# Performance work log

Hardware: AMD Instinct MI355X
Metric: run time of the kernel (lower is better)

## Reference

```python
import jax, jax.numpy as jnp
import numpy as np

D_MODEL = 1024
NUM_HEADS = 16
D_HEAD = D_MODEL // NUM_HEADS
BATCH = 4
SEQ = 2048
NEG_INF = -1e30


def setup_inputs() -> dict:
    key = jax.random.key(0)
    k_x, k_q, k_k, k_v, k_o = jax.random.split(key, 5)
    scale = 1.0 / np.sqrt(D_MODEL)
    x = jax.random.normal(k_x, (BATCH, SEQ, D_MODEL), dtype=jnp.float32)
    Qw = jax.random.normal(k_q, (D_MODEL, D_MODEL), dtype=jnp.float32) * scale
    Kw = jax.random.normal(k_k, (D_MODEL, D_MODEL), dtype=jnp.float32) * scale
    Vw = jax.random.normal(k_v, (D_MODEL, D_MODEL), dtype=jnp.float32) * scale
    Ow = jax.random.normal(k_o, (D_MODEL, D_MODEL), dtype=jnp.float32) * scale
    padding_mask = jnp.zeros((BATCH, SEQ), dtype=bool)  # True = masked position
    return {"x": x, "Qw": Qw, "Kw": Kw, "Vw": Vw, "Ow": Ow, "padding_mask": padding_mask}


def reference(x, Qw, Kw, Vw, Ow, padding_mask):
    B, S, D = x.shape
    H, dh = NUM_HEADS, D_HEAD
    # torch Linear (no bias): y = x @ W.T
    q = jnp.einsum("bsd,ed->bse", x, Qw).reshape(B, S, H, dh)
    k = jnp.einsum("bsd,ed->bse", x, Kw).reshape(B, S, H, dh)
    v = jnp.einsum("bsd,ed->bse", x, Vw).reshape(B, S, H, dh)
    # scores: [B, H, Sq, Sk]
    score = jnp.einsum("bqhd,bkhd->bhqk", q, k) / jnp.sqrt(jnp.float32(dh))
    # causal mask (masked=True)
    causal = jnp.tril(jnp.ones((S, S), dtype=bool))  # True = keep
    score = jnp.where(causal[None, None, :, :], score, NEG_INF)
    # padding mask: True = masked key position
    score = jnp.where(padding_mask[:, None, None, :], NEG_INF, score)
    attn = jax.nn.softmax(score, axis=-1)  # dropout=0.0 (eval mode)
    ctx = jnp.einsum("bhqk,bkhd->bqhd", attn, v).reshape(B, S, D)
    out = jnp.einsum("bsd,ed->bse", ctx, Ow)
    return out
```

## Files before the change

### kernel.cpp

```cpp
#include <hip/hip_runtime.h>
#include <hip/hip_bf16.h>

typedef __attribute__((ext_vector_type(8))) short short8;
typedef __attribute__((ext_vector_type(4))) float f32x4;

#define MFMA_BF16_16x16x32(a,b,c) __builtin_amdgcn_mfma_f32_16x16x32_bf16((a),(b),(c),0,0,0)

constexpr int B_  = 4;
constexpr int S_  = 2048;
constexpr int H_  = 16;
constexpr int DH_ = 64;
constexpr int D_  = 1024;
constexpr int M_  = B_ * S_;

__device__ __forceinline__ unsigned short f2bf(float f) {
  union { float f; unsigned u; } v; v.f = f;
  unsigned u = v.u;
  u += 0x7fffu + ((u >> 16) & 1u);
  return (unsigned short)(u >> 16);
}

__device__ __forceinline__ short8 cvt8(f32x4 a, f32x4 b) {
  union { __hip_bfloat162 h[4]; short8 s; } u;
  u.h[0] = __float22bfloat162_rn(make_float2(a[0], a[1]));
  u.h[1] = __float22bfloat162_rn(make_float2(a[2], a[3]));
  u.h[2] = __float22bfloat162_rn(make_float2(b[0], b[1]));
  u.h[3] = __float22bfloat162_rn(make_float2(b[2], b[3]));
  return u.s;
}

__global__ __launch_bounds__(256)
void gemm_qkv(const float* __restrict__ x,
              const float* __restrict__ Qw, const float* __restrict__ Kw,
              const float* __restrict__ Vw,
              unsigned short* __restrict__ Qo, unsigned short* __restrict__ Ko,
              unsigned short* __restrict__ VTo) {
  constexpr int BM = 128, BK = 32, LDK = 40;
  __shared__ __align__(16) short As[BM * LDK];
  __shared__ __align__(16) short Bs[BM * LDK];

  const int nb = blockIdx.x;
  const float* W;
  unsigned short* out;
  float scale = 1.0f;
  int epi;
  if (nb < 8)       { W = Qw; out = Qo;  scale = 0.125f; epi = 1; }
  else if (nb < 16) { W = Kw; out = Ko;  epi = 1; }
  else              { W = Vw; out = VTo; epi = 2; }

  const int tid  = threadIdx.x;
  const int lane = tid & 63;
  const int w    = tid >> 6;
  const int quad = lane >> 4;
  const int l16  = lane & 15;
  const int wm   = (w >> 1) * 64;
  const int wn   = (w & 1) * 64;

  const int m0 = blockIdx.y * BM;
  const int n0 = (nb & 7) * 128;

  f32x4 acc[4][4];
  #pragma unroll
  for (int i = 0; i < 4; ++i)
    #pragma unroll
    for (int j = 0; j < 4; ++j)
      acc[i][j] = (f32x4){0.f, 0.f, 0.f, 0.f};

  for (int k0 = 0; k0 < D_; k0 += BK) {
    __syncthreads();
    #pragma unroll
    for (int i = 0; i < 2; ++i) {
      int flat = i * 256 + tid;
      int row  = flat >> 2;
      int col  = (flat & 3) * 8;
      const float* Ap = x + (size_t)(m0 + row) * D_ + k0 + col;
      *(short8*)(&As[row * LDK + col]) = cvt8(*(const f32x4*)Ap, *(const f32x4*)(Ap + 4));
      const float* Wp = W + (size_t)(n0 + row) * D_ + k0 + col;
      *(short8*)(&Bs[row * LDK + col]) = cvt8(*(const f32x4*)Wp, *(const f32x4*)(Wp + 4));
    }
    __syncthreads();

    short8 af[4], bf[4];
    #pragma unroll
    for (int i = 0; i < 4; ++i)
      af[i] = *(const short8*)(&As[(wm + i * 16 + l16) * LDK + quad * 8]);
    #pragma unroll
    for (int j = 0; j < 4; ++j)
      bf[j] = *(const short8*)(&Bs[(wn + j * 16 + l16) * LDK + quad * 8]);
    #pragma unroll
    for (int i = 0; i < 4; ++i)
      #pragma unroll
      for (int j = 0; j < 4; ++j)
        acc[i][j] = MFMA_BF16_16x16x32(af[i], bf[j], acc[i][j]);
  }

  #pragma unroll
  for (int i = 0; i < 4; ++i)
    #pragma unroll
    for (int j = 0; j < 4; ++j)
      #pragma unroll
      for (int r = 0; r < 4; ++r) {
        int m = m0 + wm + i * 16 + quad * 4 + r;
        int n = n0 + wn + j * 16 + l16;
        unsigned short bv = f2bf(acc[i][j][r] * scale);
        int b = m >> 11, s = m & (S_ - 1);
        int h = n >> 6,  d = n & (DH_ - 1);
        if (epi == 1)
          out[((size_t)(b * H_ + h) * S_ + s) * DH_ + d] = bv;
        else
          out[((size_t)(b * H_ + h) * DH_ + d) * S_ + s] = bv;
      }
}

__global__ __launch_bounds__(256)
void gemm_out(const unsigned short* __restrict__ A,
              const float* __restrict__ W,
              float* __restrict__ out) {
  constexpr int BM = 128, BK = 32, LDK = 40;
  __shared__ __align__(16) short As[BM * LDK];
  __shared__ __align__(16) short Bs[BM * LDK];

  const int tid  = threadIdx.x;
  const int lane = tid & 63;
  const int w    = tid >> 6;
  const int quad = lane >> 4;
  const int l16  = lane & 15;
  const int wm   = (w >> 1) * 64;
  const int wn   = (w & 1) * 64;

  const int m0 = blockIdx.y * BM;
  const int n0 = blockIdx.x * 128;

  f32x4 acc[4][4];
  #pragma unroll
  for (int i = 0; i < 4; ++i)
    #pragma unroll
    for (int j = 0; j < 4; ++j)
      acc[i][j] = (f32x4){0.f, 0.f, 0.f, 0.f};

  for (int k0 = 0; k0 < D_; k0 += BK) {
    __syncthreads();
    #pragma unroll
    for (int i = 0; i < 2; ++i) {
      int flat = i * 256 + tid;
      int row  = flat >> 2;
      int col  = (flat & 3) * 8;
      *(short8*)(&As[row * LDK + col]) =
          *(const short8*)(A + (size_t)(m0 + row) * D_ + k0 + col);
      const float* Wp = W + (size_t)(n0 + row) * D_ + k0 + col;
      *(short8*)(&Bs[row * LDK + col]) = cvt8(*(const f32x4*)Wp, *(const f32x4*)(Wp + 4));
    }
    __syncthreads();

    short8 af[4], bf[4];
    #pragma unroll
    for (int i = 0; i < 4; ++i)
      af[i] = *(const short8*)(&As[(wm + i * 16 + l16) * LDK + quad * 8]);
    #pragma unroll
    for (int j = 0; j < 4; ++j)
      bf[j] = *(const short8*)(&Bs[(wn + j * 16 + l16) * LDK + quad * 8]);
    #pragma unroll
    for (int i = 0; i < 4; ++i)
      #pragma unroll
      for (int j = 0; j < 4; ++j)
        acc[i][j] = MFMA_BF16_16x16x32(af[i], bf[j], acc[i][j]);
  }

  #pragma unroll
  for (int i = 0; i < 4; ++i)
    #pragma unroll
    for (int j = 0; j < 4; ++j)
      #pragma unroll
      for (int r = 0; r < 4; ++r) {
        int m = m0 + wm + i * 16 + quad * 4 + r;
        int n = n0 + wn + j * 16 + l16;
        out[(size_t)m * D_ + n] = acc[i][j][r];
      }
}

__global__ __launch_bounds__(256)
void attn(const unsigned short* __restrict__ Q,
          const unsigned short* __restrict__ K,
          const unsigned short* __restrict__ VT,
          const unsigned char* __restrict__ pmask,
          unsigned short* __restrict__ CTX) {
  constexpr int LDP = 72;
  __shared__ __align__(16) short Ps[4 * 32 * LDP];

  const int tid  = threadIdx.x;
  const int lane = tid & 63;
  const int w    = tid >> 6;
  const int quad = lane >> 4;
  const int l16  = lane & 15;

  const int L    = blockIdx.x;
  const int xcd  = L & 7;
  const int slot = L >> 3;
  const int bh   = xcd + 8 * (slot & 7);
  const int xp   = slot >> 3;
  const int b    = bh >> 4;
  const int h    = bh & 15;

  const int qts0 = 2 * xp, qts1 = 63 - 2 * xp, qts2 = 2 * xp + 1, qts3 = 62 - 2 * xp;
  const int sel  = (slot + w) & 3;
  const int qt   = (sel == 0) ? qts0 : (sel == 1) ? qts1 : (sel == 2) ? qts2 : qts3;
  const int qw   = qt * 32;

  const unsigned short* Qh = Q  + ((size_t)b * H_ + h) * S_ * DH_;
  const unsigned short* Kh = K  + ((size_t)b * H_ + h) * S_ * DH_;
  const unsigned short* Vh = VT + ((size_t)b * H_ + h) * DH_ * S_;
  const unsigned char* pmb = pmask + (size_t)b * S_;
  unsigned short* CTXb = CTX + (size_t)b * S_ * D_;
  short* Pw = &Ps[w * 32 * LDP];

  const short8 ones = {0x3F80, 0x3F80, 0x3F80, 0x3F80,
                       0x3F80, 0x3F80, 0x3F80, 0x3F80};

  short8 qf[2][2];
  #pragma unroll
  for (int i = 0; i < 2; ++i)
    #pragma unroll
    for (int c = 0; c < 2; ++c)
      qf[i][c] = *(const short8*)(Qh + (size_t)(qw + i * 16 + l16) * DH_ + c * 32 + quad * 8);

  f32x4 acc[2][4];
  f32x4 lacc[2];
  #pragma unroll
  for (int i = 0; i < 2; ++i) {
    #pragma unroll
    for (int t = 0; t < 4; ++t) acc[i][t] = (f32x4){0.f, 0.f, 0.f, 0.f};
    lacc[i] = (f32x4){0.f, 0.f, 0.f, 0.f};
  }

  const int ntiles = (qt >> 1) + 1;

  for (int kt = 0; kt < ntiles; ++kt) {
    const int k0 = kt * 64;

    short8 kb[8];
    #pragma unroll
    for (int t = 0; t < 4; ++t) {
      const unsigned short* kp = Kh + (size_t)(k0 + t * 16 + l16) * DH_ + quad * 8;
      kb[t * 2]     = *(const short8*)(kp);
      kb[t * 2 + 1] = *(const short8*)(kp + 32);
    }
    unsigned char pd[4];
    #pragma unroll
    for (int t = 0; t < 4; ++t) pd[t] = pmb[k0 + t * 16 + l16];

    f32x4 sc[2][4];
    __builtin_amdgcn_s_setprio(1);
    #pragma unroll
    for (int t = 0; t < 4; ++t) {
      #pragma unroll
      for (int i = 0; i < 2; ++i) {
        f32x4 z = (f32x4){0.f, 0.f, 0.f, 0.f};
        z = MFMA_BF16_16x16x32(qf[i][0], kb[t * 2], z);
        sc[i][t] = MFMA_BF16_16x16x32(qf[i][1], kb[t * 2 + 1], z);
      }
    }
    __builtin_amdgcn_s_setprio(0);

    #pragma unroll
    for (int t = 0; t < 4; ++t) {
      float pb = pd[t] ? -1e30f : 0.f;
      #pragma unroll
      for (int i = 0; i < 2; ++i)
        #pragma unroll
        for (int r = 0; r < 4; ++r)
          sc[i][t][r] += pb;
    }
    if (k0 + 63 > qw) {
      #pragma unroll
      for (int t = 0; t < 4; ++t) {
        int key = k0 + t * 16 + l16;
        #pragma unroll
        for (int i = 0; i < 2; ++i)
          #pragma unroll
          for (int r = 0; r < 4; ++r) {
            int qrow = qw + i * 16 + quad * 4 + r;
            if (key > qrow) sc[i][t][r] = -1e30f;
          }
      }
    }
    #pragma unroll
    for (int i = 0; i < 2; ++i)
      #pragma unroll
      for (int t = 0; t < 4; ++t)
        #pragma unroll
        for (int r = 0; r < 4; ++r)
          sc[i][t][r] = __expf(sc[i][t][r]);

    #pragma unroll
    for (int i = 0; i < 2; ++i)
      #pragma unroll
      for (int t = 0; t < 4; ++t)
        #pragma unroll
        for (int r = 0; r < 4; ++r)
          Pw[(i * 16 + quad * 4 + r) * LDP + t * 16 + l16] = (short)f2bf(sc[i][t][r]);

    short8 vb[8];
    #pragma unroll
    for (int ks = 0; ks < 2; ++ks)
      #pragma unroll
      for (int t = 0; t < 4; ++t)
        vb[ks * 4 + t] = *(const short8*)(Vh + (size_t)(t * 16 + l16) * S_ +
                                          k0 + ks * 32 + quad * 8);

    __builtin_amdgcn_s_setprio(1);
    #pragma unroll
    for (int ks = 0; ks < 2; ++ks) {
      short8 pa0 = *(const short8*)(&Pw[l16 * LDP + ks * 32 + quad * 8]);
      short8 pa1 = *(const short8*)(&Pw[(16 + l16) * LDP + ks * 32 + quad * 8]);
      #pragma unroll
      for (int t = 0; t < 4; ++t) {
        acc[0][t] = MFMA_BF16_16x16x32(pa0, vb[ks * 4 + t], acc[0][t]);
        acc[1][t] = MFMA_BF16_16x16x32(pa1, vb[ks * 4 + t], acc[1][t]);
      }
      lacc[0] = MFMA_BF16_16x16x32(pa0, ones, lacc[0]);
      lacc[1] = MFMA_BF16_16x16x32(pa1, ones, lacc[1]);
    }
    __builtin_amdgcn_s_setprio(0);
  }

  #pragma unroll
  for (int i = 0; i < 2; ++i)
    #pragma unroll
    for (int r = 0; r < 4; ++r) {
      int qrow = qw + i * 16 + quad * 4 + r;
      float inv = 1.0f / lacc[i][r];
      #pragma unroll
      for (int t = 0; t < 4; ++t)
        CTXb[(size_t)qrow * D_ + h * DH_ + t * 16 + l16] = f2bf(acc[i][t][r] * inv);
    }
}

extern "C" void kernel_launch(void* const* d_in, const int* in_sizes, int n_in,
                              void* d_out, int out_size, void* d_ws, size_t ws_size,
                              hipStream_t stream) {
  const float* x  = (const float*)d_in[0];
  const float* Qw = (const float*)d_in[1];
  const float* Kw = (const float*)d_in[2];
  const float* Vw = (const float*)d_in[3];
  const float* Ow = (const float*)d_in[4];
  const unsigned char* pm = (const unsigned char*)d_in[5];

  const size_t NE = (size_t)M_ * D_;
  unsigned short* Qall  = (unsigned short*)d_out;
  unsigned short* CTXa  = (unsigned short*)d_out + NE;
  unsigned short* Kall  = (unsigned short*)d_ws;
  unsigned short* VTall = (unsigned short*)d_ws + NE;

  gemm_qkv<<<dim3(24, M_ / 128), 256, 0, stream>>>(x, Qw, Kw, Vw,
                                                   Qall, Kall, VTall);

  attn<<<dim3(1024), 256, 0, stream>>>(Qall, Kall, VTall, pm, CTXa);

  hipMemcpyAsync(d_ws, (const void*)CTXa, NE * sizeof(unsigned short),
                 hipMemcpyDeviceToDevice, stream);

  gemm_out<<<dim3(D_ / 128, M_ / 128), 256, 0, stream>>>((unsigned short*)d_ws,
                                                         Ow, (float*)d_out);
}
```

Before: 405.4 us.

## Balance causal attention per wave by splitting long q-tile KV range across waves

The attention kernel now uses 2-wave blocks. Each block pairs a short q-tile p with a long q-tile 63-p. Wave 0 processes the whole short tile plus the first part of the long tile's KV range, and wave 1 processes the rest of it. The partial accumulators and row sums are merged through LDS behind a barrier, so both waves do about 17 KV tiles each. This targets the per-wave load imbalance of the old 4-wave scheme, where each wave handled a single causal tile of very different length. The cost is an LDS reduction, a __syncthreads, and more blocks with fewer waves each.

```diff
diff --git a/kernel.cpp b/kernel.cpp
--- a/kernel.cpp
+++ b/kernel.cpp
@@ -178,63 +178,18 @@
       }
 }
 
-__global__ __launch_bounds__(256)
-void attn(const unsigned short* __restrict__ Q,
-          const unsigned short* __restrict__ K,
-          const unsigned short* __restrict__ VT,
-          const unsigned char* __restrict__ pmask,
-          unsigned short* __restrict__ CTX) {
-  constexpr int LDP = 72;
-  __shared__ __align__(16) short Ps[4 * 32 * LDP];
-
-  const int tid  = threadIdx.x;
-  const int lane = tid & 63;
-  const int w    = tid >> 6;
-  const int quad = lane >> 4;
-  const int l16  = lane & 15;
-
-  const int L    = blockIdx.x;
-  const int xcd  = L & 7;
-  const int slot = L >> 3;
-  const int bh   = xcd + 8 * (slot & 7);
-  const int xp   = slot >> 3;
-  const int b    = bh >> 4;
-  const int h    = bh & 15;
-
-  const int qts0 = 2 * xp, qts1 = 63 - 2 * xp, qts2 = 2 * xp + 1, qts3 = 62 - 2 * xp;
-  const int sel  = (slot + w) & 3;
-  const int qt   = (sel == 0) ? qts0 : (sel == 1) ? qts1 : (sel == 2) ? qts2 : qts3;
-  const int qw   = qt * 32;
-
-  const unsigned short* Qh = Q  + ((size_t)b * H_ + h) * S_ * DH_;
-  const unsigned short* Kh = K  + ((size_t)b * H_ + h) * S_ * DH_;
-  const unsigned short* Vh = VT + ((size_t)b * H_ + h) * DH_ * S_;
-  const unsigned char* pmb = pmask + (size_t)b * S_;
-  unsigned short* CTXb = CTX + (size_t)b * S_ * D_;
-  short* Pw = &Ps[w * 32 * LDP];
-
+constexpr int LDP_ = 72;
+
+__device__ __forceinline__ void attn_range(
+    const unsigned short* __restrict__ Kh,
+    const unsigned short* __restrict__ Vh,
+    const unsigned char* __restrict__ pmb,
+    short* __restrict__ Pw,
+    const short8 qf[2][2], f32x4 acc[2][4], f32x4 lacc[2],
+    int qw, int kt0, int kt1, int quad, int l16) {
   const short8 ones = {0x3F80, 0x3F80, 0x3F80, 0x3F80,
                        0x3F80, 0x3F80, 0x3F80, 0x3F80};
-
-  short8 qf[2][2];
-  #pragma unroll
-  for (int i = 0; i < 2; ++i)
-    #pragma unroll
-    for (int c = 0; c < 2; ++c)
-      qf[i][c] = *(const short8*)(Qh + (size_t)(qw + i * 16 + l16) * DH_ + c * 32 + quad * 8);
-
-  f32x4 acc[2][4];
-  f32x4 lacc[2];
-  #pragma unroll
-  for (int i = 0; i < 2; ++i) {
-    #pragma unroll
-    for (int t = 0; t < 4; ++t) acc[i][t] = (f32x4){0.f, 0.f, 0.f, 0.f};
-    lacc[i] = (f32x4){0.f, 0.f, 0.f, 0.f};
-  }
-
-  const int ntiles = (qt >> 1) + 1;
-
-  for (int kt = 0; kt < ntiles; ++kt) {
+  for (int kt = kt0; kt < kt1; ++kt) {
     const int k0 = kt * 64;
 
     short8 kb[8];
@@ -297,7 +252,7 @@
       for (int t = 0; t < 4; ++t)
         #pragma unroll
         for (int r = 0; r < 4; ++r)
-          Pw[(i * 16 + quad * 4 + r) * LDP + t * 16 + l16] = (short)f2bf(sc[i][t][r]);
+          Pw[(i * 16 + quad * 4 + r) * LDP_ + t * 16 + l16] = (short)f2bf(sc[i][t][r]);
 
     short8 vb[8];
     #pragma unroll
@@ -310,8 +265,8 @@
     __builtin_amdgcn_s_setprio(1);
     #pragma unroll
     for (int ks = 0; ks < 2; ++ks) {
-      short8 pa0 = *(const short8*)(&Pw[l16 * LDP + ks * 32 + quad * 8]);
-      short8 pa1 = *(const short8*)(&Pw[(16 + l16) * LDP + ks * 32 + quad * 8]);
+      short8 pa0 = *(const short8*)(&Pw[l16 * LDP_ + ks * 32 + quad * 8]);
+      short8 pa1 = *(const short8*)(&Pw[(16 + l16) * LDP_ + ks * 32 + quad * 8]);
       #pragma unroll
       for (int t = 0; t < 4; ++t) {
         acc[0][t] = MFMA_BF16_16x16x32(pa0, vb[ks * 4 + t], acc[0][t]);
@@ -322,17 +277,137 @@
     }
     __builtin_amdgcn_s_setprio(0);
   }
-
-  #pragma unroll
-  for (int i = 0; i < 2; ++i)
-    #pragma unroll
-    for (int r = 0; r < 4; ++r) {
-      int qrow = qw + i * 16 + quad * 4 + r;
-      float inv = 1.0f / lacc[i][r];
+}
+
+__global__ __launch_bounds__(128)
+void attn(const unsigned short* __restrict__ Q,
+          const unsigned short* __restrict__ K,
+          const unsigned short* __restrict__ VT,
+          const unsigned char* __restrict__ pmask,
+          unsigned short* __restrict__ CTX) {
+  __shared__ __align__(16) short Ps[2 * 32 * LDP_];
+  __shared__ float Rbuf[64 * 40];
+
+  const int tid  = threadIdx.x;
+  const int lane = tid & 63;
+  const int w    = tid >> 6;
+  const int quad = lane >> 4;
+  const int l16  = lane & 15;
+
+  const int L    = blockIdx.x;
+  const int xcd  = L & 7;
+  const int slot = L >> 3;
+  const int bh   = xcd + 8 * (slot & 7);
+  const int p    = slot >> 3;
+  const int b    = bh >> 4;
+  const int h    = bh & 15;
+
+  const int qtA = p, qtB = 63 - p;
+  const int ntA = (qtA >> 1) + 1;
+  const int ntB = (qtB >> 1) + 1;
+  const int splitB = 17 - ntA;
+
+  const unsigned short* Qh = Q  + ((size_t)b * H_ + h) * S_ * DH_;
+  const unsigned short* Kh = K  + ((size_t)b * H_ + h) * S_ * DH_;
+  const unsigned short* Vh = VT + ((size_t)b * H_ + h) * DH_ * S_;
+  const unsigned char* pmb = pmask + (size_t)b * S_;
+  unsigned short* CTXb = CTX + (size_t)b * S_ * D_;
+  short* Pw = &Ps[w * 32 * LDP_];
+
+  f32x4 acc[2][4];
+  f32x4 lacc[2];
+  short8 qf[2][2];
+
+  if (w == 0) {
+    {
+      const int qw = qtA * 32;
+      #pragma unroll
+      for (int i = 0; i < 2; ++i)
+        #pragma unroll
+        for (int c = 0; c < 2; ++c)
+          qf[i][c] = *(const short8*)(Qh + (size_t)(qw + i * 16 + l16) * DH_ + c * 32 + quad * 8);
+      #pragma unroll
+      for (int i = 0; i < 2; ++i) {
+        #pragma unroll
+        for (int t = 0; t < 4; ++t) acc[i][t] = (f32x4){0.f, 0.f, 0.f, 0.f};
+        lacc[i] = (f32x4){0.f, 0.f, 0.f, 0.f};
+      }
+      attn_range(Kh, Vh, pmb, Pw, qf, acc, lacc, qw, 0, ntA, quad, l16);
+      #pragma unroll
+      for (int i = 0; i < 2; ++i)
+        #pragma unroll
+        for (int r = 0; r < 4; ++r) {
+          int qrow = qw + i * 16 + quad * 4 + r;
+          float inv = 1.0f / lacc[i][r];
+          #pragma unroll
+          for (int t = 0; t < 4; ++t)
+            CTXb[(size_t)qrow * D_ + h * DH_ + t * 16 + l16] = f2bf(acc[i][t][r] * inv);
+        }
+    }
+    {
+      const int qw = qtB * 32;
+      #pragma unroll
+      for (int i = 0; i < 2; ++i)
+        #pragma unroll
+        for (int c = 0; c < 2; ++c)
+          qf[i][c] = *(const short8*)(Qh + (size_t)(qw + i * 16 + l16) * DH_ + c * 32 + quad * 8);
+      #pragma unroll
+      for (int i = 0; i < 2; ++i) {
+        #pragma unroll
+        for (int t = 0; t < 4; ++t) acc[i][t] = (f32x4){0.f, 0.f, 0.f, 0.f};
+        lacc[i] = (f32x4){0.f, 0.f, 0.f, 0.f};
+      }
+      attn_range(Kh, Vh, pmb, Pw, qf, acc, lacc, qw, 0, splitB, quad, l16);
+      __syncthreads();
+      #pragma unroll
+      for (int i = 0; i < 2; ++i) {
+        #pragma unroll
+        for (int t = 0; t < 4; ++t)
+          #pragma unroll
+          for (int r = 0; r < 4; ++r)
+            acc[i][t][r] += Rbuf[lane * 40 + i * 16 + t * 4 + r];
+        #pragma unroll
+        for (int r = 0; r < 4; ++r)
+          lacc[i][r] += Rbuf[lane * 40 + 32 + i * 4 + r];
+      }
+      #pragma unroll
+      for (int i = 0; i < 2; ++i)
+        #pragma unroll
+        for (int r = 0; r < 4; ++r) {
+          int qrow = qw + i * 16 + quad * 4 + r;
+          float inv = 1.0f / lacc[i][r];
+          #pragma unroll
+          for (int t = 0; t < 4; ++t)
+            CTXb[(size_t)qrow * D_ + h * DH_ + t * 16 + l16] = f2bf(acc[i][t][r] * inv);
+        }
+    }
+  } else {
+    const int qw = qtB * 32;
+    #pragma unroll
+    for (int i = 0; i < 2; ++i)
+      #pragma unroll
+      for (int c = 0; c < 2; ++c)
+        qf[i][c] = *(const short8*)(Qh + (size_t)(qw + i * 16 + l16) * DH_ + c * 32 + quad * 8);
+    #pragma unroll
+    for (int i = 0; i < 2; ++i) {
+      #pragma unroll
+      for (int t = 0; t < 4; ++t) acc[i][t] = (f32x4){0.f, 0.f, 0.f, 0.f};
+      lacc[i] = (f32x4){0.f, 0.f, 0.f, 0.f};
+    }
+    attn_range(Kh, Vh, pmb, Pw, qf, acc, lacc, qw, splitB, ntB, quad, l16);
+    #pragma unroll
+    for (int i = 0; i < 2; ++i) {
       #pragma unroll
       for (int t = 0; t < 4; ++t)
-        CTXb[(size_t)qrow * D_ + h * DH_ + t * 16 + l16] = f2bf(acc[i][t][r] * inv);
-    }
+        #pragma unroll
+        for (int r = 0; r < 4; ++r)
+          Rbuf[lane * 40 + i * 16 + t * 4 + r] = acc[i][t][r];
+      #pragma unroll
+      for (int r = 0; r < 4; ++r)
+        Rbuf[lane * 40 + 32 + i * 4 + r] = lacc[i][r];
+    }
+    __syncthreads();
+  }
 }
 
 extern "C" void kernel_launch(void* const* d_in, const int* in_sizes, int n_in,
@@ -354,7 +429,7 @@
   gemm_qkv<<<dim3(24, M_ / 128), 256, 0, stream>>>(x, Qw, Kw, Vw,
                                                    Qall, Kall, VTall);
 
-  attn<<<dim3(1024), 256, 0, stream>>>(Qall, Kall, VTall, pm, CTXa);
+  attn<<<dim3(2048), 128, 0, stream>>>(Qall, Kall, VTall, pm, CTXa);
 
   hipMemcpyAsync(d_ws, (const void*)CTXa, NE * sizeof(unsigned short),
                  hipMemcpyDeviceToDevice, stream);
```

Measured after the change: 374.1 us. 7.7% less time.
